# Performance work log

Hardware: AMD Instinct MI355X
Metric: run time of the kernel (lower is better)

## Reference

```python
import jax, jax.numpy as jnp
import numpy as np

D_MODEL = 1024
N_HEADS = 16
MAX_LAG = 512
D_K = D_MODEL // N_HEADS


def setup_inputs() -> dict:
    key = jax.random.key(0)
    ks = jax.random.split(key, 11)
    B, S = 2, 2048
    x = jax.random.normal(ks[0], (B, S, D_MODEL), dtype=jnp.float32)
    lag = jax.random.randint(ks[1], (S,), 0, MAX_LAG + 1, dtype=jnp.int64)
    scale = 1.0 / np.sqrt(D_MODEL)
    wq = jax.random.normal(ks[2], (D_MODEL, D_MODEL), dtype=jnp.float32) * scale
    bq = jnp.zeros((D_MODEL,), dtype=jnp.float32)
    wk = jax.random.normal(ks[3], (D_MODEL, D_MODEL), dtype=jnp.float32) * scale
    bk = jnp.zeros((D_MODEL,), dtype=jnp.float32)
    wv = jax.random.normal(ks[4], (D_MODEL, D_MODEL), dtype=jnp.float32) * scale
    bv = jnp.zeros((D_MODEL,), dtype=jnp.float32)
    wo = jax.random.normal(ks[5], (D_MODEL, D_MODEL), dtype=jnp.float32) * scale
    bo = jnp.zeros((D_MODEL,), dtype=jnp.float32)
    lag_bias = jax.random.normal(ks[6], (N_HEADS, MAX_LAG + 1), dtype=jnp.float32) * 0.02
    return {"x": x, "lag": lag, "wq": wq, "bq": bq, "wk": wk, "bk": bk,
            "wv": wv, "bv": bv, "wo": wo, "bo": bo, "lag_bias": lag_bias}


def reference(x, lag, wq, bq, wk, bk, wv, bv, wo, bo, lag_bias):
    B, S, D = x.shape
    H, dk = N_HEADS, D_K
    # projections: torch Linear is x @ W.T + b; here weights stored as (in, out)
    q = (x @ wq + bq).reshape(B, S, H, dk).transpose(0, 2, 1, 3)  # (B,H,S,dk)
    k = (x @ wk + bk).reshape(B, S, H, dk).transpose(0, 2, 1, 3)
    v = (x @ wv + bv).reshape(B, S, H, dk).transpose(0, 2, 1, 3)
    scores = jnp.einsum('bhqd,bhkd->bhqk', q, k) / jnp.sqrt(jnp.float32(dk))
    ld = jnp.abs(lag[:, None] - lag[None, :]).astype(jnp.int32)  # (S,S)
    bias = lag_bias[:, ld]  # (H,S,S)
    attn = jax.nn.softmax(scores + bias[None], axis=-1)
    out = jnp.einsum('bhqk,bhkd->bhqd', attn, v)
    out = out.transpose(0, 2, 1, 3).reshape(B, S, D)
    return out @ wo + bo
```

## Files before the change

kernel.cpp:

```cpp
#include <hip/hip_runtime.h>

typedef __bf16 bf16;
typedef __bf16 bf16x8 __attribute__((ext_vector_type(8)));
typedef float f32x4 __attribute__((ext_vector_type(4)));

__device__ __forceinline__ f32x4 mfma16(bf16x8 a, bf16x8 b, f32x4 c) {
  return __builtin_amdgcn_mfma_f32_16x16x32_bf16(a, b, c, 0, 0, 0);
}
__device__ __forceinline__ void gload16(const bf16* g, bf16* l) {
  __builtin_amdgcn_global_load_lds((const __attribute__((address_space(1))) unsigned int*)g,
                                   (__attribute__((address_space(3))) unsigned int*)l, 16, 0, 0);
}

__global__ __launch_bounds__(256) void cvt_x_kernel(const float* __restrict__ in,
                                                    bf16* __restrict__ out, int n8) {
  int i = blockIdx.x * 256 + threadIdx.x;
  if (i >= n8) return;
  const float4* p = (const float4*)in + (size_t)i * 2;
  float4 f0 = p[0], f1 = p[1];
  bf16x8 o;
  o[0] = (bf16)f0.x; o[1] = (bf16)f0.y; o[2] = (bf16)f0.z; o[3] = (bf16)f0.w;
  o[4] = (bf16)f1.x; o[5] = (bf16)f1.y; o[6] = (bf16)f1.z; o[7] = (bf16)f1.w;
  *((bf16x8*)out + i) = o;
}

__global__ __launch_bounds__(256) void cvt_wt_kernel(const float* __restrict__ in,
                                                     bf16* __restrict__ out) {
  __shared__ float t[64][68];
  int bx = blockIdx.x & 15;
  int by = blockIdx.x >> 4;
  int tid = threadIdx.x;
  int r = tid >> 2, p = tid & 3;
  const float* src = in + (size_t)(by * 64 + r) * 1024 + bx * 64 + p * 16;
#pragma unroll
  for (int j = 0; j < 16; j += 4)
    *(float4*)&t[r][p * 16 + j] = *(const float4*)(src + j);
  __syncthreads();
  int n = tid >> 2, sp = tid & 3;
  bf16 tmp[16];
#pragma unroll
  for (int j = 0; j < 16; ++j) tmp[j] = (bf16)t[sp * 16 + j][n];
  bf16* dst = out + (size_t)(bx * 64 + n) * 1024 + by * 64 + sp * 16;
  *(bf16x8*)dst = *(bf16x8*)&tmp[0];
  *(bf16x8*)(dst + 8) = *(bf16x8*)&tmp[8];
}

__global__ void cvt_bias_kernel(const float* __restrict__ bq, const float* __restrict__ bk,
                                const float* __restrict__ bv, float* __restrict__ out) {
  int i = blockIdx.x * 256 + threadIdx.x;
  if (i < 1024) out[i] = bq[i];
  else if (i < 2048) out[i] = bk[i - 1024];
  else if (i < 3072) out[i] = bv[i - 2048];
}

__global__ __launch_bounds__(256) void sort_lag_kernel(const int* __restrict__ lag,
                                                       int* __restrict__ perm,
                                                       int* __restrict__ slag) {
  __shared__ int l[2048];
  int tid = threadIdx.x;
  for (int i = tid; i < 2048; i += 256) l[i] = lag[i];
  __syncthreads();
  int i = blockIdx.x * 32 + (tid >> 3);
  int s = tid & 7;
  int vi = l[i];
  int cnt = 0;
  for (int j = s * 256; j < s * 256 + 256; j += 4) {
    int4 vj = *(const int4*)&l[j];
    cnt += (vj.x < vi || (vj.x == vi && (j + 0) < i));
    cnt += (vj.y < vi || (vj.y == vi && (j + 1) < i));
    cnt += (vj.z < vi || (vj.z == vi && (j + 2) < i));
    cnt += (vj.w < vi || (vj.w == vi && (j + 3) < i));
  }
  cnt += __shfl_xor(cnt, 1);
  cnt += __shfl_xor(cnt, 2);
  cnt += __shfl_xor(cnt, 4);
  if (s == 0) { perm[cnt] = i; slag[cnt] = vi; }
}

__global__ __launch_bounds__(256) void pack_kv_kernel(const bf16* __restrict__ qkv,
                                                      const int* __restrict__ perm,
                                                      bf16* __restrict__ kp,
                                                      bf16* __restrict__ vt) {
  __shared__ bf16 t[64][72];
  int blk = blockIdx.x;
  int st = blk & 31, h = (blk >> 5) & 15, b = blk >> 9;
  int tid = threadIdx.x;
  int r = tid >> 2, p = tid & 3;
  int src_s = perm[st * 64 + r];
  {
    const bf16* src = qkv + (size_t)(b * 2048 + src_s) * 3072 + 1024 + h * 64 + p * 16;
    bf16* dst = kp + (size_t)((b * 16 + h) * 2048 + st * 64 + r) * 64 + p * 16;
    *(bf16x8*)dst = *(const bf16x8*)src;
    *(bf16x8*)(dst + 8) = *(const bf16x8*)(src + 8);
  }
  {
    const bf16* src = qkv + (size_t)(b * 2048 + src_s) * 3072 + 2048 + h * 64 + p * 16;
    *(bf16x8*)&t[r][p * 16] = *(const bf16x8*)src;
    *(bf16x8*)&t[r][p * 16 + 8] = *(const bf16x8*)(src + 8);
    __syncthreads();
    int d = tid >> 2, sp = tid & 3;
    bf16 tmp[16];
#pragma unroll
    for (int j = 0; j < 16; ++j) tmp[j] = t[sp * 16 + j][d];
    bf16* dst = vt + (size_t)((b * 16 + h) * 64 + d) * 2048 + st * 64 + sp * 16;
    *(bf16x8*)dst = *(bf16x8*)&tmp[0];
    *(bf16x8*)(dst + 8) = *(bf16x8*)&tmp[8];
  }
}

template <int OUT_BF16>
__global__ __launch_bounds__(256) void gemm_bt_kernel(
    const bf16* __restrict__ A, const bf16* __restrict__ Bt,
    const float* __restrict__ bias, void* __restrict__ C,
    int M, int N, int K, int scale_cols, float scale_val) {
  __shared__ __align__(16) bf16 As[128 * 64];
  __shared__ __align__(16) bf16 Bs[128 * 64];
  int bn = blockIdx.x * 128, bm = blockIdx.y * 128;
  int tid = threadIdx.x;
  int l = tid & 63;
  int w = tid >> 6;
  int wr = w >> 1, wc = w & 1;
  int g = l >> 4, c = l & 15;
  int swz = (c & 7) << 3;
  int srow = l >> 3;
  int scol = ((l & 7) ^ srow) << 3;
  const bf16* Ap = A + (size_t)(bm + w * 32 + srow) * K + scol;
  const bf16* Bp = Bt + (size_t)(bn + w * 32 + srow) * K + scol;
  bf16* AsW = As + w * 32 * 64;
  bf16* BsW = Bs + w * 32 * 64;

  f32x4 acc[4][4] = {};
  for (int k0 = 0; k0 < K; k0 += 64) {
    __syncthreads();
#pragma unroll
    for (int i = 0; i < 4; ++i) {
      gload16(Ap + (size_t)(8 * i) * K + k0, AsW + i * 512);
      gload16(Bp + (size_t)(8 * i) * K + k0, BsW + i * 512);
    }
    __syncthreads();
#pragma unroll
    for (int kh = 0; kh < 2; ++kh) {
      bf16x8 af[4], bfr[4];
#pragma unroll
      for (int m = 0; m < 4; ++m)
        af[m] = *(const bf16x8*)&As[(wr * 64 + m * 16 + c) * 64 + ((kh * 32 + g * 8) ^ swz)];
#pragma unroll
      for (int n = 0; n < 4; ++n)
        bfr[n] = *(const bf16x8*)&Bs[(wc * 64 + n * 16 + c) * 64 + ((kh * 32 + g * 8) ^ swz)];
#pragma unroll
      for (int m = 0; m < 4; ++m)
#pragma unroll
        for (int n = 0; n < 4; ++n)
          acc[m][n] = mfma16(af[m], bfr[n], acc[m][n]);
    }
  }
  int rowb = bm + wr * 64;
  int colb = bn + wc * 64;
#pragma unroll
  for (int n = 0; n < 4; ++n) {
    int col = colb + n * 16 + c;
    float bv = bias[col];
    float s = (col < scale_cols) ? scale_val : 1.0f;
#pragma unroll
    for (int m = 0; m < 4; ++m) {
      int row = rowb + m * 16 + g * 4;
#pragma unroll
      for (int j = 0; j < 4; ++j) {
        float v = (acc[m][n][j] + bv) * s;
        if (OUT_BF16)
          ((bf16*)C)[(size_t)(row + j) * N + col] = (bf16)v;
        else
          ((float*)C)[(size_t)(row + j) * N + col] = v;
      }
    }
  }
}

__global__ __launch_bounds__(256) void attn_kernel(
    const bf16* __restrict__ qkv, const bf16* __restrict__ kp,
    const bf16* __restrict__ vt, const int* __restrict__ lag,
    const int* __restrict__ slag, const float* __restrict__ lag_bias,
    bf16* __restrict__ out) {
  __shared__ __align__(16) bf16 Ks0[64 * 64];
  __shared__ __align__(16) bf16 Vs0[64 * 64];
  __shared__ __align__(16) bf16 Ks1[64 * 64];
  __shared__ __align__(16) bf16 Vs1[64 * 64];
  __shared__ __align__(16) bf16 Ps[4][32][72];
  __shared__ float bias_s[516];
  __shared__ int lag_s[2048];

  int blk = blockIdx.x;
  blk = (blk & 7) * 64 + (blk >> 3);
  int qt = blk & 15;
  int h = (blk >> 4) & 15;
  int b = blk >> 8;
  int tid = threadIdx.x;
  int w = tid >> 6, l = tid & 63, g = l >> 4, c = l & 15;

  for (int i = tid; i < 513; i += 256) bias_s[i] = lag_bias[h * 513 + i] * 1.44269504f;
  for (int i = tid; i < 2048; i += 256) lag_s[i] = slag[i];

  int q0 = qt * 128 + w * 32;
  const bf16* qbase = qkv + (size_t)(b * 2048 + q0) * 3072 + h * 64;
  bf16x8 qf[2][2];
#pragma unroll
  for (int m = 0; m < 2; ++m)
#pragma unroll
    for (int kh = 0; kh < 2; ++kh)
      qf[m][kh] = *(const bf16x8*)(qbase + (size_t)(m * 16 + c) * 3072 + kh * 32 + g * 8);

  int lagq[2][4];
#pragma unroll
  for (int m = 0; m < 2; ++m)
#pragma unroll
    for (int j = 0; j < 4; ++j) lagq[m][j] = lag[q0 + m * 16 + g * 4 + j];

  int swz = (c & 7) << 3;
  int off0 = (g * 8) ^ swz;
  int off1 = off0 ^ 32;

  int r0 = w * 16 + (l >> 3);
  int colE = ((l & 7) ^ (l >> 3)) << 3;
  const bf16* kbase = kp + (size_t)(b * 16 + h) * 2048 * 64;
  const bf16* vbase = vt + (size_t)(b * 16 + h) * 64 * 2048;
  const bf16* kg0 = kbase + (size_t)r0 * 64 + colE;
  const bf16* kg1 = kbase + (size_t)(r0 + 8) * 64 + colE;
  const bf16* vg0 = vbase + (size_t)r0 * 2048 + colE;
  const bf16* vg1 = vbase + (size_t)(r0 + 8) * 2048 + colE;

#define STAGE(KD, VD)                    \
  do {                                   \
    gload16(kg0, KD + w * 1024);         \
    gload16(kg1, KD + w * 1024 + 512);   \
    gload16(vg0, VD + w * 1024);         \
    gload16(vg1, VD + w * 1024 + 512);   \
    kg0 += 64 * 64; kg1 += 64 * 64;      \
    vg0 += 64; vg1 += 64;                \
  } while (0)

  STAGE(Ks0, Vs0);
  __syncthreads();

  f32x4 oacc[2][4] = {};
  float psum[2][4] = {};

#define TILE(KB, VB, KT)                                                          \
  do {                                                                            \
    f32x4 sf[2][4] = {};                                                          \
    int lagk[4];                                                                  \
    _Pragma("unroll") for (int kb = 0; kb < 4; ++kb) {                            \
      int row = kb * 16 + c;                                                      \
      bf16x8 k0 = *(const bf16x8*)&KB[row * 64 + off0];                           \
      bf16x8 k1 = *(const bf16x8*)&KB[row * 64 + off1];                           \
      sf[0][kb] = mfma16(qf[0][0], k0, sf[0][kb]);                                \
      sf[0][kb] = mfma16(qf[0][1], k1, sf[0][kb]);                                \
      sf[1][kb] = mfma16(qf[1][0], k0, sf[1][kb]);                                \
      sf[1][kb] = mfma16(qf[1][1], k1, sf[1][kb]);                                \
      lagk[kb] = lag_s[(KT) + kb * 16 + c];                                       \
    }                                                                             \
    _Pragma("unroll") for (int m = 0; m < 2; ++m)                                 \
    _Pragma("unroll") for (int kb = 0; kb < 4; ++kb)                              \
    _Pragma("unroll") for (int j = 0; j < 4; ++j) {                               \
      int ld = lagq[m][j] - lagk[kb];                                             \
      ld = ld < 0 ? -ld : ld;                                                     \
      float p = __builtin_amdgcn_exp2f(sf[m][kb][j] + bias_s[ld]);                \
      psum[m][j] += p;                                                            \
      Ps[w][m * 16 + g * 4 + j][kb * 16 + c] = (bf16)p;                           \
    }                                                                             \
    asm volatile("s_waitcnt lgkmcnt(0)" ::: "memory");                            \
    _Pragma("unroll") for (int ph = 0; ph < 2; ++ph) {                            \
      bf16x8 pa0 = *(const bf16x8*)&Ps[w][c][ph * 32 + g * 8];                    \
      bf16x8 pa1 = *(const bf16x8*)&Ps[w][16 + c][ph * 32 + g * 8];               \
      int voff = ph ? off1 : off0;                                                \
      _Pragma("unroll") for (int n = 0; n < 4; ++n) {                             \
        bf16x8 vf = *(const bf16x8*)&VB[(n * 16 + c) * 64 + voff];                \
        oacc[0][n] = mfma16(pa0, vf, oacc[0][n]);                                 \
        oacc[1][n] = mfma16(pa1, vf, oacc[1][n]);                                 \
      }                                                                           \
    }                                                                             \
  } while (0)

  for (int kt = 0; kt < 2048; kt += 128) {
    if (kt + 64 < 2048) STAGE(Ks1, Vs1);
    TILE(Ks0, Vs0, kt);
    __syncthreads();
    if (kt + 128 < 2048) STAGE(Ks0, Vs0);
    TILE(Ks1, Vs1, kt + 64);
    __syncthreads();
  }

#pragma unroll
  for (int m = 0; m < 2; ++m) {
#pragma unroll
    for (int j = 0; j < 4; ++j) {
      float s = psum[m][j];
      s += __shfl_xor(s, 1);
      s += __shfl_xor(s, 2);
      s += __shfl_xor(s, 4);
      s += __shfl_xor(s, 8);
      float inv = 1.f / s;
      bf16* ob = out + (size_t)(b * 2048 + q0 + m * 16 + g * 4 + j) * 1024 + h * 64;
#pragma unroll
      for (int n = 0; n < 4; ++n)
        ob[n * 16 + c] = (bf16)(oacc[m][n][j] * inv);
    }
  }
#undef STAGE
#undef TILE
}

extern "C" void kernel_launch(void* const* d_in, const int* in_sizes, int n_in,
                              void* d_out, int out_size, void* d_ws, size_t ws_size,
                              hipStream_t stream) {
  const float* x        = (const float*)d_in[0];
  const int*   lag      = (const int*)d_in[1];
  const float* wq       = (const float*)d_in[2];
  const float* bq       = (const float*)d_in[3];
  const float* wk       = (const float*)d_in[4];
  const float* bk       = (const float*)d_in[5];
  const float* wv       = (const float*)d_in[6];
  const float* bv       = (const float*)d_in[7];
  const float* wo       = (const float*)d_in[8];
  const float* bo       = (const float*)d_in[9];
  const float* lag_bias = (const float*)d_in[10];

  char* ws = (char*)d_ws;
  bf16*  xb    = (bf16*)ws;
  bf16*  wqkvt = (bf16*)(ws + (8u  << 20));
  bf16*  wot   = (bf16*)(ws + (14u << 20));
  float* bqkv  = (float*)(ws + (16u << 20));
  int*   perm  = (int*)(ws + (16u << 20) + 32768);
  int*   slag  = (int*)(ws + (16u << 20) + 65536);
  bf16*  qkv   = (bf16*)(ws + (17u << 20));
  bf16*  vtb   = (bf16*)(ws + (41u << 20));
  bf16*  aout  = (bf16*)(ws + (49u << 20));
  bf16*  kpk   = xb;

  sort_lag_kernel<<<64, 256, 0, stream>>>(lag, perm, slag);
  cvt_x_kernel<<<2048, 256, 0, stream>>>(x, xb, 524288);
  cvt_wt_kernel<<<256, 256, 0, stream>>>(wq, wqkvt);
  cvt_wt_kernel<<<256, 256, 0, stream>>>(wk, wqkvt + (1u << 20));
  cvt_wt_kernel<<<256, 256, 0, stream>>>(wv, wqkvt + (2u << 20));
  cvt_wt_kernel<<<256, 256, 0, stream>>>(wo, wot);
  cvt_bias_kernel<<<12, 256, 0, stream>>>(bq, bk, bv, bqkv);
  gemm_bt_kernel<1><<<dim3(24, 32), 256, 0, stream>>>(
      xb, wqkvt, bqkv, qkv, 4096, 3072, 1024, 1024, 0.125f * 1.44269504f);
  pack_kv_kernel<<<1024, 256, 0, stream>>>(qkv, perm, kpk, vtb);
  attn_kernel<<<512, 256, 0, stream>>>(qkv, kpk, vtb, lag, slag, lag_bias, aout);
  gemm_bt_kernel<0><<<dim3(8, 32), 256, 0, stream>>>(
      aout, wot, bo, (float*)d_out, 4096, 1024, 1024, 0, 1.0f);
}
```

Measured before the change: 182.0 us.

## Halve attention query tile per block and fuse weight/bias conversion launches

The attention kernel now processes 16 query rows per wave (64 per block) instead of 32, doubling the grid to 1024 blocks. This raises parallelism and occupancy but halves K/V reuse per staged tile. Separately, the four weight-transpose launches and the bias-copy launch are merged into one kernel to cut launch overhead. The block index remapping is updated to match the new tile count.

```diff
diff --git a/kernel.cpp b/kernel.cpp
--- a/kernel.cpp
+++ b/kernel.cpp
@@ -24,12 +24,27 @@
   *((bf16x8*)out + i) = o;
 }
 
-__global__ __launch_bounds__(256) void cvt_wt_kernel(const float* __restrict__ in,
-                                                     bf16* __restrict__ out) {
+__global__ __launch_bounds__(256) void cvt_wtb_kernel(
+    const float* __restrict__ wq, const float* __restrict__ wk,
+    const float* __restrict__ wv, const float* __restrict__ wo,
+    const float* __restrict__ bq, const float* __restrict__ bk,
+    const float* __restrict__ bv, bf16* __restrict__ wqkvt,
+    bf16* __restrict__ wot, float* __restrict__ bqkv) {
+  int blk = blockIdx.x;
+  int tid = threadIdx.x;
+  if (blk >= 1024) {
+    int i = (blk - 1024) * 256 + tid;
+    if (i < 1024) bqkv[i] = bq[i];
+    else if (i < 2048) bqkv[i] = bk[i - 1024];
+    else if (i < 3072) bqkv[i] = bv[i - 2048];
+    return;
+  }
   __shared__ float t[64][68];
-  int bx = blockIdx.x & 15;
-  int by = blockIdx.x >> 4;
-  int tid = threadIdx.x;
+  int wsel = blk >> 8, sub = blk & 255;
+  const float* in = wsel == 0 ? wq : wsel == 1 ? wk : wsel == 2 ? wv : wo;
+  bf16* out = (wsel == 3) ? wot : (wqkvt + (size_t)wsel * (1u << 20));
+  int bx = sub & 15;
+  int by = sub >> 4;
   int r = tid >> 2, p = tid & 3;
   const float* src = in + (size_t)(by * 64 + r) * 1024 + bx * 64 + p * 16;
 #pragma unroll
@@ -43,14 +58,6 @@
   bf16* dst = out + (size_t)(bx * 64 + n) * 1024 + by * 64 + sp * 16;
   *(bf16x8*)dst = *(bf16x8*)&tmp[0];
   *(bf16x8*)(dst + 8) = *(bf16x8*)&tmp[8];
-}
-
-__global__ void cvt_bias_kernel(const float* __restrict__ bq, const float* __restrict__ bk,
-                                const float* __restrict__ bv, float* __restrict__ out) {
-  int i = blockIdx.x * 256 + threadIdx.x;
-  if (i < 1024) out[i] = bq[i];
-  else if (i < 2048) out[i] = bk[i - 1024];
-  else if (i < 3072) out[i] = bv[i - 2048];
 }
 
 __global__ __launch_bounds__(256) void sort_lag_kernel(const int* __restrict__ lag,
@@ -185,35 +192,30 @@
   __shared__ __align__(16) bf16 Vs0[64 * 64];
   __shared__ __align__(16) bf16 Ks1[64 * 64];
   __shared__ __align__(16) bf16 Vs1[64 * 64];
-  __shared__ __align__(16) bf16 Ps[4][32][72];
+  __shared__ __align__(16) bf16 Ps[4][16][72];
   __shared__ float bias_s[516];
   __shared__ int lag_s[2048];
 
   int blk = blockIdx.x;
-  blk = (blk & 7) * 64 + (blk >> 3);
-  int qt = blk & 15;
-  int h = (blk >> 4) & 15;
-  int b = blk >> 8;
+  blk = (blk & 7) * 128 + (blk >> 3);
+  int qt = blk & 31;
+  int h = (blk >> 5) & 15;
+  int b = blk >> 9;
   int tid = threadIdx.x;
   int w = tid >> 6, l = tid & 63, g = l >> 4, c = l & 15;
 
   for (int i = tid; i < 513; i += 256) bias_s[i] = lag_bias[h * 513 + i] * 1.44269504f;
   for (int i = tid; i < 2048; i += 256) lag_s[i] = slag[i];
 
-  int q0 = qt * 128 + w * 32;
+  int q0 = qt * 64 + w * 16;
   const bf16* qbase = qkv + (size_t)(b * 2048 + q0) * 3072 + h * 64;
-  bf16x8 qf[2][2];
-#pragma unroll
-  for (int m = 0; m < 2; ++m)
-#pragma unroll
-    for (int kh = 0; kh < 2; ++kh)
-      qf[m][kh] = *(const bf16x8*)(qbase + (size_t)(m * 16 + c) * 3072 + kh * 32 + g * 8);
-
-  int lagq[2][4];
-#pragma unroll
-  for (int m = 0; m < 2; ++m)
-#pragma unroll
-    for (int j = 0; j < 4; ++j) lagq[m][j] = lag[q0 + m * 16 + g * 4 + j];
+  bf16x8 qf[2];
+  qf[0] = *(const bf16x8*)(qbase + (size_t)c * 3072 + g * 8);
+  qf[1] = *(const bf16x8*)(qbase + (size_t)c * 3072 + 32 + g * 8);
+
+  int lagq[4];
+#pragma unroll
+  for (int j = 0; j < 4; ++j) lagq[j] = lag[q0 + g * 4 + j];
 
   int swz = (c & 7) << 3;
   int off0 = (g * 8) ^ swz;
@@ -241,42 +243,38 @@
   STAGE(Ks0, Vs0);
   __syncthreads();
 
-  f32x4 oacc[2][4] = {};
-  float psum[2][4] = {};
+  f32x4 oacc[4] = {};
+  float psum[4] = {0.f, 0.f, 0.f, 0.f};
 
 #define TILE(KB, VB, KT)                                                          \
   do {                                                                            \
-    f32x4 sf[2][4] = {};                                                          \
+    f32x4 sf[4] = {};                                                             \
     int lagk[4];                                                                  \
     _Pragma("unroll") for (int kb = 0; kb < 4; ++kb) {                            \
       int row = kb * 16 + c;                                                      \
       bf16x8 k0 = *(const bf16x8*)&KB[row * 64 + off0];                           \
       bf16x8 k1 = *(const bf16x8*)&KB[row * 64 + off1];                           \
-      sf[0][kb] = mfma16(qf[0][0], k0, sf[0][kb]);                                \
-      sf[0][kb] = mfma16(qf[0][1], k1, sf[0][kb]);                                \
-      sf[1][kb] = mfma16(qf[1][0], k0, sf[1][kb]);                                \
-      sf[1][kb] = mfma16(qf[1][1], k1, sf[1][kb]);                                \
+      sf[kb] = mfma16(qf[0], k0, sf[kb]);                                         \
+      sf[kb] = mfma16(qf[1], k1, sf[kb]);                                         \
       lagk[kb] = lag_s[(KT) + kb * 16 + c];                                       \
     }                                                                             \
-    _Pragma("unroll") for (int m = 0; m < 2; ++m)                                 \
     _Pragma("unroll") for (int kb = 0; kb < 4; ++kb)                              \
     _Pragma("unroll") for (int j = 0; j < 4; ++j) {                               \
-      int ld = lagq[m][j] - lagk[kb];                                             \
+      int ld = lagq[j] - lagk[kb];                                                \
       ld = ld < 0 ? -ld : ld;                                                     \
-      float p = __builtin_amdgcn_exp2f(sf[m][kb][j] + bias_s[ld]);                \
-      psum[m][j] += p;                                                            \
-      Ps[w][m * 16 + g * 4 + j][kb * 16 + c] = (bf16)p;                           \
+      float p = __builtin_amdgcn_exp2f(sf[kb][j] + bias_s[ld]);                   \
+      psum[j] += p;                                                               \
+      Ps[w][g * 4 + j][kb * 16 + c] = (bf16)p;                                    \
     }                                                                             \
     asm volatile("s_waitcnt lgkmcnt(0)" ::: "memory");                            \
-    _Pragma("unroll") for (int ph = 0; ph < 2; ++ph) {                            \
-      bf16x8 pa0 = *(const bf16x8*)&Ps[w][c][ph * 32 + g * 8];                    \
-      bf16x8 pa1 = *(const bf16x8*)&Ps[w][16 + c][ph * 32 + g * 8];               \
-      int voff = ph ? off1 : off0;                                                \
-      _Pragma("unroll") for (int n = 0; n < 4; ++n) {                             \
-        bf16x8 vf = *(const bf16x8*)&VB[(n * 16 + c) * 64 + voff];                \
-        oacc[0][n] = mfma16(pa0, vf, oacc[0][n]);                                 \
-        oacc[1][n] = mfma16(pa1, vf, oacc[1][n]);                                 \
-      }                                                                           \
+    bf16x8 pa0 = *(const bf16x8*)&Ps[w][c][g * 8];                                \
+    bf16x8 pa1 = *(const bf16x8*)&Ps[w][c][32 + g * 8];                           \
+    _Pragma("unroll") for (int n = 0; n < 4; ++n) {                               \
+      int row = n * 16 + c;                                                       \
+      bf16x8 v0 = *(const bf16x8*)&VB[row * 64 + off0];                           \
+      bf16x8 v1 = *(const bf16x8*)&VB[row * 64 + off1];                           \
+      oacc[n] = mfma16(pa0, v0, oacc[n]);                                         \
+      oacc[n] = mfma16(pa1, v1, oacc[n]);                                         \
     }                                                                             \
   } while (0)
 
@@ -290,20 +288,17 @@
   }
 
 #pragma unroll
-  for (int m = 0; m < 2; ++m) {
-#pragma unroll
-    for (int j = 0; j < 4; ++j) {
-      float s = psum[m][j];
-      s += __shfl_xor(s, 1);
-      s += __shfl_xor(s, 2);
-      s += __shfl_xor(s, 4);
-      s += __shfl_xor(s, 8);
-      float inv = 1.f / s;
-      bf16* ob = out + (size_t)(b * 2048 + q0 + m * 16 + g * 4 + j) * 1024 + h * 64;
-#pragma unroll
-      for (int n = 0; n < 4; ++n)
-        ob[n * 16 + c] = (bf16)(oacc[m][n][j] * inv);
-    }
+  for (int j = 0; j < 4; ++j) {
+    float s = psum[j];
+    s += __shfl_xor(s, 1);
+    s += __shfl_xor(s, 2);
+    s += __shfl_xor(s, 4);
+    s += __shfl_xor(s, 8);
+    float inv = 1.f / s;
+    bf16* ob = out + (size_t)(b * 2048 + q0 + g * 4 + j) * 1024 + h * 64;
+#pragma unroll
+    for (int n = 0; n < 4; ++n)
+      ob[n * 16 + c] = (bf16)(oacc[n][j] * inv);
   }
 #undef STAGE
 #undef TILE
@@ -338,15 +333,11 @@
 
   sort_lag_kernel<<<64, 256, 0, stream>>>(lag, perm, slag);
   cvt_x_kernel<<<2048, 256, 0, stream>>>(x, xb, 524288);
-  cvt_wt_kernel<<<256, 256, 0, stream>>>(wq, wqkvt);
-  cvt_wt_kernel<<<256, 256, 0, stream>>>(wk, wqkvt + (1u << 20));
-  cvt_wt_kernel<<<256, 256, 0, stream>>>(wv, wqkvt + (2u << 20));
-  cvt_wt_kernel<<<256, 256, 0, stream>>>(wo, wot);
-  cvt_bias_kernel<<<12, 256, 0, stream>>>(bq, bk, bv, bqkv);
+  cvt_wtb_kernel<<<1036, 256, 0, stream>>>(wq, wk, wv, wo, bq, bk, bv, wqkvt, wot, bqkv);
   gemm_bt_kernel<1><<<dim3(24, 32), 256, 0, stream>>>(
       xb, wqkvt, bqkv, qkv, 4096, 3072, 1024, 1024, 0.125f * 1.44269504f);
   pack_kv_kernel<<<1024, 256, 0, stream>>>(qkv, perm, kpk, vtb);
-  attn_kernel<<<512, 256, 0, stream>>>(qkv, kpk, vtb, lag, slag, lag_bias, aout);
+  attn_kernel<<<1024, 256, 0, stream>>>(qkv, kpk, vtb, lag, slag, lag_bias, aout);
   gemm_bt_kernel<0><<<dim3(8, 32), 256, 0, stream>>>(
       aout, wot, bo, (float*)d_out, 4096, 1024, 1024, 0, 1.0f);
 }
```

After: 179.5 us. About the same (-1.4%).
